# Optimization experiments

Hardware: AMD Instinct MI355X
Metric: run time of the kernel (lower is better)

## Reference

```python
import jax, jax.numpy as jnp
import numpy as np

RANK = 4
ALPHA = 4.0
SCALE = ALPHA / RANK


def setup_inputs() -> dict:
    key = jax.random.key(0)
    k1, k2, k3, k4 = jax.random.split(key, 4)
    B, S, H = 4, 2048, 2048
    NH, HD = 16, 128
    x = jax.random.normal(k1, (B, S, H), dtype=jnp.float32)
    W_orig = jax.random.normal(k2, (H, NH, HD), dtype=jnp.float32) * (1.0 / np.sqrt(H))
    A_kernel = jax.random.normal(k3, (H, RANK), dtype=jnp.float32) * (1.0 / RANK)
    # B kernel is zero-init in the module; use small randn so the LoRA path is exercised
    B_kernel = jax.random.normal(k4, (RANK, NH, HD), dtype=jnp.float32) * 0.02
    return {"x": x, "W_orig": W_orig, "A_kernel": A_kernel, "B_kernel": B_kernel}


def reference(x, W_orig, A_kernel, B_kernel):
    # original layer: EinsumDense 'abc,cde->abde'  [B,S,H] x [H,NH,HD] -> [B,S,NH,HD]
    original_output = jnp.einsum('bsc,chd->bshd', x, W_orig)
    # LoRA path: Dense to rank, then EinsumDense back up, scaled
    ax = x @ A_kernel                                   # [B,S,r]
    lora_output = jnp.einsum('bsr,rhd->bshd', ax, B_kernel) * SCALE
    return original_output + lora_output
```

## Files before the change

### kernel.cpp

```cpp
#include <hip/hip_runtime.h>
#include <hip/hip_bf16.h>
#include <cstdint>


using bf16 = __hip_bfloat16;
typedef __attribute__((ext_vector_type(8))) __bf16 bf16x8;
typedef __attribute__((ext_vector_type(4))) float f32x4;

constexpr int Mdim = 8192;
constexpr int Ndim = 2048;
constexpr int Kdim = 2048;
constexpr float SCALE = 1.0f;

constexpr int BM = 128, BN = 128, BK = 64;
constexpr int CVT_BLOCKS = (Mdim * Kdim) / (256 * 8);
constexpr int PREP_BLOCKS = (Ndim / 64) * (Kdim / 64);

__device__ __forceinline__ void gload_lds16(const void* g, void* l) {
  __builtin_amdgcn_global_load_lds(
      (const __attribute__((address_space(1))) uint32_t*)g,
      (__attribute__((address_space(3))) uint32_t*)l,
      16, 0, 0);
}

__global__ void prep_all(const float* __restrict__ X,
                         const float* __restrict__ W,
                         const float* __restrict__ A,
                         const float* __restrict__ Bk,
                         uint16_t* __restrict__ Xb,
                         uint16_t* __restrict__ Wt) {
  __shared__ float tile[64][65];

  if (blockIdx.x < CVT_BLOCKS) {
    const int i = blockIdx.x * blockDim.x + threadIdx.x;
    const float4* Xv = (const float4*)X;
    float4 a = Xv[i * 2 + 0];
    float4 b = Xv[i * 2 + 1];
    uint16_t o[8];
    o[0] = __bfloat16_as_ushort(__float2bfloat16(a.x));
    o[1] = __bfloat16_as_ushort(__float2bfloat16(a.y));
    o[2] = __bfloat16_as_ushort(__float2bfloat16(a.z));
    o[3] = __bfloat16_as_ushort(__float2bfloat16(a.w));
    o[4] = __bfloat16_as_ushort(__float2bfloat16(b.x));
    o[5] = __bfloat16_as_ushort(__float2bfloat16(b.y));
    o[6] = __bfloat16_as_ushort(__float2bfloat16(b.z));
    o[7] = __bfloat16_as_ushort(__float2bfloat16(b.w));
    *reinterpret_cast<uint4*>(Xb + (size_t)i * 8) = *reinterpret_cast<uint4*>(o);
  } else {
    const int pid = blockIdx.x - CVT_BLOCKS;
    const int tx = threadIdx.x & 63;
    const int ty = threadIdx.x >> 6;
    const int n0 = (pid & 31) * 64, k0 = (pid >> 5) * 64;

    const int n = n0 + tx;
    const float b0 = Bk[0 * Ndim + n];
    const float b1 = Bk[1 * Ndim + n];
    const float b2 = Bk[2 * Ndim + n];
    const float b3 = Bk[3 * Ndim + n];

    for (int i = ty; i < 64; i += 4) {
      const int k = k0 + i;
      float w = W[(size_t)k * Ndim + n];
      w += SCALE * (A[k * 4 + 0] * b0 + A[k * 4 + 1] * b1 +
                    A[k * 4 + 2] * b2 + A[k * 4 + 3] * b3);
      tile[tx][i] = w;
    }
    __syncthreads();
    for (int i = ty; i < 64; i += 4) {
      Wt[(size_t)(n0 + i) * Kdim + (k0 + tx)] =
          __bfloat16_as_ushort(__float2bfloat16(tile[i][tx]));
    }
  }
}

__global__ void gemm_bt(const uint16_t* __restrict__ X,
                        const uint16_t* __restrict__ Wt,
                        float* __restrict__ out) {
  __shared__ uint16_t As[BM * BK];
  __shared__ uint16_t Bs[BN * BK];

  const int t = threadIdx.x;
  const int wave = t >> 6, lane = t & 63;

  const int lid = blockIdx.x;
  const int s   = lid >> 3;
  const int bx  = s & 15;
  const int by  = (lid & 7) * 8 + (s >> 4);
  const int m0 = by * BM, n0 = bx * BN;

  const int wm = wave & 1, wn = wave >> 1;
  const int l15 = lane & 15, kg = lane >> 4;
  const int sw = l15 & 7;

  const int r8 = lane >> 3;
  const int gc = (lane & 7) ^ r8;
  const uint16_t* Ag = X + (size_t)m0 * Kdim;
  const uint16_t* Bg = Wt + (size_t)n0 * Kdim;

  f32x4 acc[4][4] = {};

  for (int kt = 0; kt < Kdim; kt += BK) {
#pragma unroll
    for (int c = 0; c < 4; ++c) {
      const int ch = wave * 4 + c;
      const int row = ch * 8 + r8;
      gload_lds16(Ag + (size_t)row * Kdim + kt + gc * 8, &As[ch * 512]);
      gload_lds16(Bg + (size_t)row * Kdim + kt + gc * 8, &Bs[ch * 512]);
    }
    __syncthreads();

#pragma unroll
    for (int s2 = 0; s2 < 2; ++s2) {
      bf16x8 af[4], bfr[4];
      const int p = (s2 * 4 + kg) ^ sw;
#pragma unroll
      for (int i = 0; i < 4; ++i) {
        const int ra = wm * 64 + i * 16 + l15;
        const int rb = wn * 64 + i * 16 + l15;
        af[i]  = *reinterpret_cast<const bf16x8*>(&As[ra * BK + p * 8]);
        bfr[i] = *reinterpret_cast<const bf16x8*>(&Bs[rb * BK + p * 8]);
      }
#pragma unroll
      for (int i = 0; i < 4; ++i)
#pragma unroll
        for (int j = 0; j < 4; ++j)
          acc[i][j] = __builtin_amdgcn_mfma_f32_16x16x32_bf16(af[i], bfr[j], acc[i][j], 0, 0, 0);
    }
    __syncthreads();
  }

#pragma unroll
  for (int i = 0; i < 4; ++i) {
    const int m_base = m0 + wm * 64 + i * 16 + kg * 4;
#pragma unroll
    for (int j = 0; j < 4; ++j) {
      const int n = n0 + wn * 64 + j * 16 + l15;
#pragma unroll
      for (int r = 0; r < 4; ++r) {
        out[(size_t)(m_base + r) * Ndim + n] = acc[i][j][r];
      }
    }
  }
}

extern "C" void kernel_launch(void* const* d_in, const int* in_sizes, int n_in,
                              void* d_out, int out_size, void* d_ws, size_t ws_size,
                              hipStream_t stream) {
  const float* x  = (const float*)d_in[0];
  const float* W  = (const float*)d_in[1];
  const float* A  = (const float*)d_in[2];
  const float* Bk = (const float*)d_in[3];
  float* out = (float*)d_out;

  uint16_t* Xb = (uint16_t*)d_ws;
  uint16_t* Wt = (uint16_t*)((char*)d_ws + (size_t)Mdim * Kdim * 2);

  prep_all<<<CVT_BLOCKS + PREP_BLOCKS, 256, 0, stream>>>(x, W, A, Bk, Xb, Wt);

  gemm_bt<<<(Ndim / BN) * (Mdim / BM), 256, 0, stream>>>(Xb, Wt, out);
}
```

Measured before the change: 199.7 us.

## Replace GEMM with 256x256 double-buffered 8-phase pipelined kernel

Replaces the 128x128 single-buffered GEMM with a 256x256 tile, 512-thread kernel. It double-buffers the tiles in 128 KB of LDS and interleaves global-to-LDS staging with eight MFMA phases per two K-steps. The phases are ordered by explicit vmcnt/lgkmcnt waits, barriers and setprio. The aim is to hide load latency behind compute and to raise data reuse per tile, with XCD-aware block mapping. The cost is heavier register and LDS use, and hand-tuned wait counts that are fragile to get right.

```diff
diff --git a/kernel.cpp b/kernel.cpp
--- a/kernel.cpp
+++ b/kernel.cpp
@@ -12,7 +12,8 @@
 constexpr int Kdim = 2048;
 constexpr float SCALE = 1.0f;
 
-constexpr int BM = 128, BN = 128, BK = 64;
+constexpr int BM = 256, BN = 256, BK = 64;
+constexpr int NT2 = Kdim / (2 * BK);
 constexpr int CVT_BLOCKS = (Mdim * Kdim) / (256 * 8);
 constexpr int PREP_BLOCKS = (Ndim / 64) * (Kdim / 64);
 
@@ -73,74 +74,167 @@
   }
 }
 
-__global__ void gemm_bt(const uint16_t* __restrict__ X,
-                        const uint16_t* __restrict__ Wt,
-                        float* __restrict__ out) {
-  __shared__ uint16_t As[BM * BK];
-  __shared__ uint16_t Bs[BN * BK];
+#define FENCE() asm volatile("" ::: "memory")
+#define VMW(N)  asm volatile("s_waitcnt vmcnt(" #N ")" ::: "memory")
+#define PMID()                                                                 \
+  do {                                                                         \
+    FENCE();                                                                   \
+    __builtin_amdgcn_s_barrier();                                              \
+    asm volatile("s_waitcnt lgkmcnt(0)" ::: "memory");                         \
+  } while (0)
+#define PEND()                                                                 \
+  do {                                                                         \
+    FENCE();                                                                   \
+    __builtin_amdgcn_s_barrier();                                              \
+    FENCE();                                                                   \
+  } while (0)
+
+__global__ __launch_bounds__(512, 2) void gemm_8ph(
+    const uint16_t* __restrict__ X, const uint16_t* __restrict__ Wt,
+    float* __restrict__ out) {
+  __shared__ uint16_t lds[65536];
 
   const int t = threadIdx.x;
   const int wave = t >> 6, lane = t & 63;
-
-  const int lid = blockIdx.x;
-  const int s   = lid >> 3;
-  const int bx  = s & 15;
-  const int by  = (lid & 7) * 8 + (s >> 4);
-  const int m0 = by * BM, n0 = bx * BN;
-
-  const int wm = wave & 1, wn = wave >> 1;
+  const int wm = wave >> 2, wn = wave & 3;
   const int l15 = lane & 15, kg = lane >> 4;
   const int sw = l15 & 7;
 
+  const int lid = blockIdx.x;
+  const int xcd = lid & 7, loc = lid >> 3;
+  const int by = xcd * 4 + (loc & 3);
+  const int bx = loc >> 2;
+  const int m0 = by * BM, n0 = bx * BN;
+
+  const uint16_t* Ag = X + (size_t)m0 * Kdim;
+  const uint16_t* Bg = Wt + (size_t)n0 * Kdim;
+
   const int r8 = lane >> 3;
   const int gc = (lane & 7) ^ r8;
-  const uint16_t* Ag = X + (size_t)m0 * Kdim;
-  const uint16_t* Bg = Wt + (size_t)n0 * Kdim;
-
-  f32x4 acc[4][4] = {};
-
-  for (int kt = 0; kt < Kdim; kt += BK) {
-#pragma unroll
-    for (int c = 0; c < 4; ++c) {
-      const int ch = wave * 4 + c;
-      const int row = ch * 8 + r8;
-      gload_lds16(Ag + (size_t)row * Kdim + kt + gc * 8, &As[ch * 512]);
-      gload_lds16(Bg + (size_t)row * Kdim + kt + gc * 8, &Bs[ch * 512]);
-    }
-    __syncthreads();
-
-#pragma unroll
-    for (int s2 = 0; s2 < 2; ++s2) {
-      bf16x8 af[4], bfr[4];
-      const int p = (s2 * 4 + kg) ^ sw;
-#pragma unroll
-      for (int i = 0; i < 4; ++i) {
-        const int ra = wm * 64 + i * 16 + l15;
-        const int rb = wn * 64 + i * 16 + l15;
-        af[i]  = *reinterpret_cast<const bf16x8*>(&As[ra * BK + p * 8]);
-        bfr[i] = *reinterpret_cast<const bf16x8*>(&Bs[rb * BK + p * 8]);
-      }
-#pragma unroll
-      for (int i = 0; i < 4; ++i)
-#pragma unroll
-        for (int j = 0; j < 4; ++j)
-          acc[i][j] = __builtin_amdgcn_mfma_f32_16x16x32_bf16(af[i], bfr[j], acc[i][j], 0, 0, 0);
-    }
-    __syncthreads();
-  }
-
-#pragma unroll
-  for (int i = 0; i < 4; ++i) {
-    const int m_base = m0 + wm * 64 + i * 16 + kg * 4;
-#pragma unroll
-    for (int j = 0; j < 4; ++j) {
-      const int n = n0 + wn * 64 + j * 16 + l15;
+  const int slot0 = wave * 2, slot1 = slot0 + 1;
+  const size_t go0 = (size_t)(slot0 * 8 + r8) * Kdim + gc * 8;
+  const size_t go1 = (size_t)(slot1 * 8 + r8) * Kdim + gc * 8;
+
+  int aE[2], bE[2];
+#pragma unroll
+  for (int s2 = 0; s2 < 2; ++s2) {
+    const int p = (s2 * 4 + kg) ^ sw;
+    aE[s2] = (wm * 64 + l15) * 64 + p * 8;
+    bE[s2] = (wn * 32 + l15) * 64 + p * 8;
+  }
+
+#define STAGE_A(buf, h, kt)                                                    \
+  do {                                                                         \
+    gload_lds16(Ag + go0 + (size_t)(h) * 128 * Kdim + (kt),                    \
+                &lds[(buf) * 32768 + (h) * 8192 + slot0 * 512]);               \
+    gload_lds16(Ag + go1 + (size_t)(h) * 128 * Kdim + (kt),                    \
+                &lds[(buf) * 32768 + (h) * 8192 + slot1 * 512]);               \
+  } while (0)
+#define STAGE_B(buf, h, kt)                                                    \
+  do {                                                                         \
+    gload_lds16(Bg + go0 + (size_t)(h) * 128 * Kdim + (kt),                    \
+                &lds[(buf) * 32768 + 16384 + (h) * 8192 + slot0 * 512]);       \
+    gload_lds16(Bg + go1 + (size_t)(h) * 128 * Kdim + (kt),                    \
+                &lds[(buf) * 32768 + 16384 + (h) * 8192 + slot1 * 512]);       \
+  } while (0)
+
+  bf16x8 a[4][2], b[2][2];
+  f32x4 acc[8][4] = {};
+
+#define READ_A(QM, buf)                                                        \
+  do {                                                                         \
+    _Pragma("unroll") for (int ii = 0; ii < 4; ++ii)                           \
+        _Pragma("unroll") for (int s2 = 0; s2 < 2; ++s2)                       \
+            a[ii][s2] = *reinterpret_cast<const bf16x8*>(                      \
+                &lds[(buf) * 32768 + (QM) * 8192 + ii * 1024 + aE[s2]]);       \
+  } while (0)
+#define READ_B(QN, buf)                                                        \
+  do {                                                                         \
+    _Pragma("unroll") for (int jj = 0; jj < 2; ++jj)                           \
+        _Pragma("unroll") for (int s2 = 0; s2 < 2; ++s2)                       \
+            b[jj][s2] = *reinterpret_cast<const bf16x8*>(                      \
+                &lds[(buf) * 32768 + 16384 + (QN) * 8192 + jj * 1024 +         \
+                     bE[s2]]);                                                 \
+  } while (0)
+#define MMA(QM, QN)                                                            \
+  do {                                                                         \
+    __builtin_amdgcn_s_setprio(1);                                             \
+    _Pragma("unroll") for (int s2 = 0; s2 < 2; ++s2)                           \
+        _Pragma("unroll") for (int ii = 0; ii < 4; ++ii)                       \
+            _Pragma("unroll") for (int jj = 0; jj < 2; ++jj)                   \
+                acc[(QM) * 4 + ii][(QN) * 2 + jj] =                            \
+                    __builtin_amdgcn_mfma_f32_16x16x32_bf16(                   \
+                        a[ii][s2], b[jj][s2],                                  \
+                        acc[(QM) * 4 + ii][(QN) * 2 + jj], 0, 0, 0);           \
+    __builtin_amdgcn_s_setprio(0);                                             \
+  } while (0)
+
+  STAGE_A(0, 0, 0); STAGE_B(0, 0, 0); STAGE_A(0, 1, 0); STAGE_B(0, 1, 0);
+  FENCE();
+  STAGE_A(1, 0, BK); STAGE_B(1, 0, BK); STAGE_A(1, 1, BK);
+  FENCE();
+  VMW(6);
+  __builtin_amdgcn_s_barrier();
+  FENCE();
+
+#pragma unroll 1
+  for (int j = 0; j < NT2; ++j) {
+    const int kt1 = j * 128 + 64;
+    const int kn0 = j * 128 + 128;
+    const int kn1 = j * 128 + 192;
+    const bool full = (j < NT2 - 1);
+
+    STAGE_B(1, 1, kt1);
+    VMW(8);
+    READ_A(0, 0); READ_B(0, 0);
+    PMID(); MMA(0, 0); PEND();
+
+    if (full) STAGE_A(0, 0, kn0);
+    READ_B(1, 0);
+    PMID(); MMA(0, 1); PEND();
+
+    READ_A(1, 0); READ_B(0, 0);
+    PMID(); MMA(1, 0); PEND();
+
+    if (full) { STAGE_B(0, 0, kn0); STAGE_A(0, 1, kn0); VMW(8); }
+    else      { VMW(2); }
+    READ_B(1, 0);
+    PMID(); MMA(1, 1); PEND();
+
+    if (full) { STAGE_B(0, 1, kn0); VMW(8); }
+    else      { VMW(0); }
+    READ_A(0, 1); READ_B(0, 1);
+    PMID(); MMA(0, 0); PEND();
+
+    if (full) STAGE_A(1, 0, kn1);
+    READ_B(1, 1);
+    PMID(); MMA(0, 1); PEND();
+
+    READ_A(1, 1); READ_B(0, 1);
+    PMID(); MMA(1, 0); PEND();
+
+    if (full) { STAGE_B(1, 0, kn1); STAGE_A(1, 1, kn1); VMW(8); }
+    READ_B(1, 1);
+    PMID(); MMA(1, 1); PEND();
+  }
+
+#pragma unroll
+  for (int i = 0; i < 8; ++i) {
+    const int mb = m0 + (i >> 2) * 128 + wm * 64 + (i & 3) * 16 + kg * 4;
+#pragma unroll
+    for (int jn = 0; jn < 4; ++jn) {
+      const int n = n0 + (jn >> 1) * 128 + wn * 32 + (jn & 1) * 16 + l15;
 #pragma unroll
       for (int r = 0; r < 4; ++r) {
-        out[(size_t)(m_base + r) * Ndim + n] = acc[i][j][r];
+        out[(size_t)(mb + r) * Ndim + n] = acc[i][jn][r];
       }
     }
   }
+#undef STAGE_A
+#undef STAGE_B
+#undef READ_A
+#undef READ_B
+#undef MMA
 }
 
 extern "C" void kernel_launch(void* const* d_in, const int* in_sizes, int n_in,
@@ -157,5 +251,5 @@
 
   prep_all<<<CVT_BLOCKS + PREP_BLOCKS, 256, 0, stream>>>(x, W, A, Bk, Xb, Wt);
 
-  gemm_bt<<<(Ndim / BN) * (Mdim / BM), 256, 0, stream>>>(Xb, Wt, out);
-}
+  gemm_8ph<<<(Mdim / BM) * (Ndim / BN), 512, 0, stream>>>(Xb, Wt, out);
+}
```

After: 197.2 us. About the same (-1.3%).
